# Optimization experiments

Measured on AMD Instinct MI355X. Metric: run time of the kernel, lower is better.

## Reference

```python
import jax, jax.numpy as jnp
import numpy as np

VOXEL_SIZE = jnp.array([0.075, 0.075], dtype=jnp.float32)
PC_RANGE = jnp.array([-54.0, -54.0], dtype=jnp.float32)
FUSION_STRIDE = 8.0
SRC_STRIDES = (4.0, 8.0)
RADII = (2.4, 4.8)
NSAMPLE = 16
NKEY = 500


def _mlp(x, w1, g1, b1, w2, b2):
    # Linear(no bias) + BatchNorm(eval, running mean=0/var=1 -> affine) + ReLU, then Linear
    h = jax.nn.relu((x @ w1) * g1 + b1)
    return h @ w2 + b2


def _world(coords, stride):
    # voxel coord -> world xy center
    return (coords.astype(jnp.float32) + 0.5) * stride * VOXEL_SIZE + PC_RANGE


def _gather_rows(x, idx):
    # x: (B, N, ...), idx: (B, ...) -> per-batch row gather
    return jax.vmap(lambda f, i: f[i])(x, idx)


def _knn(key_world, src_world, src_feat, radius):
    # key_world (B,Nk,2), src_world (B,Ns,2), src_feat (B,Ns,C)
    d2 = jnp.sum((key_world[:, :, None, :] - src_world[:, None, :, :]) ** 2, axis=-1)  # (B,Nk,Ns)
    d2 = jnp.where(d2 <= radius * radius, d2, jnp.inf)
    negd, idx = jax.lax.top_k(-d2, NSAMPLE)  # nearest NSAMPLE within radius, (B,Nk,K)
    valid = jnp.isfinite(negd).astype(src_feat.dtype)  # empty==0 mask
    feats = _gather_rows(src_feat, idx)  # (B,Nk,K,C)
    return feats * valid[..., None]


def setup_inputs() -> dict:
    key = jax.random.key(0)
    ks = jax.random.split(key, 24)
    s = 0.05
    return {
        'fusion_feat': jax.random.normal(ks[0], (2, 20000, 128), jnp.float32),
        'src_feat_a': jax.random.normal(ks[1], (2, 30000, 128), jnp.float32),
        'src_feat_b': jax.random.normal(ks[2], (2, 30000, 128), jnp.float32),
        'heat_w1': jax.random.normal(ks[3], (128, 128), jnp.float32) * s,
        'heat_g1': jnp.ones((128,), jnp.float32),
        'heat_b1': jnp.zeros((128,), jnp.float32),
        'heat_w2': jax.random.normal(ks[4], (128, 10), jnp.float32) * s,
        'heat_b2': jnp.zeros((10,), jnp.float32),
        'knn_w': jax.random.normal(ks[5], (2, 16), jnp.float32) * s,
        'knn_b': jnp.zeros((2,), jnp.float32),
        'kw_w1': jax.random.normal(ks[6], (128, 64), jnp.float32) * s,
        'kw_g1': jnp.ones((64,), jnp.float32),
        'kw_b1': jnp.zeros((64,), jnp.float32),
        'kw_w2': jax.random.normal(ks[7], (64, 3), jnp.float32) * s,
        'kw_b2': jnp.zeros((3,), jnp.float32),
        'fuse_w1': jax.random.normal(ks[8], (256, 256), jnp.float32) * s,
        'fuse_g1': jnp.ones((256,), jnp.float32),
        'fuse_b1': jnp.zeros((256,), jnp.float32),
        'fuse_w2': jax.random.normal(ks[9], (256, 128), jnp.float32) * s,
        'fuse_b2': jnp.zeros((128,), jnp.float32),
        'fusion_coords': jax.random.randint(ks[10], (2, 20000, 2), 0, 180, jnp.int32),
        'src_coords_a': jax.random.randint(ks[11], (2, 30000, 2), 0, 360, jnp.int32),
        'src_coords_b': jax.random.randint(ks[12], (2, 30000, 2), 0, 180, jnp.int32),
    }


def reference(fusion_feat, src_feat_a, src_feat_b, heat_w1, heat_g1, heat_b1,
              heat_w2, heat_b2, knn_w, knn_b, kw_w1, kw_g1, kw_b1, kw_w2, kw_b2,
              fuse_w1, fuse_g1, fuse_b1, fuse_w2, fuse_b2,
              fusion_coords, src_coords_a, src_coords_b):
    B = fusion_feat.shape[0]
    # heatmap head over all fusion voxels
    scores10 = _mlp(fusion_feat, heat_w1, heat_g1, heat_b1, heat_w2, heat_b2)  # (B,Nf,10)
    heat_scores = jnp.max(scores10, axis=-1)
    cls = jnp.argmax(scores10, axis=-1)
    # per-sample top-k key voxel selection
    _, tki = jax.lax.top_k(jax.nn.sigmoid(heat_scores), NKEY)  # (B,Nk)
    key_feat = _gather_rows(fusion_feat, tki)      # (B,Nk,128)
    key_coords = _gather_rows(fusion_coords, tki)  # (B,Nk,2)
    key_class = _gather_rows(cls, tki)             # (B,Nk)
    key_world = _world(key_coords, FUSION_STRIDE)  # (B,Nk,2)

    srcs = ((src_feat_a, src_coords_a), (src_feat_b, src_coords_b))
    mlp_feats = []
    for s, (sf, sc) in enumerate(srcs):
        sw = _world(sc, SRC_STRIDES[s])
        kf = _knn(key_world, sw, sf, RADII[s])  # (B,Nk,K,C), zeroed where empty
        # Linear over the K neighbor axis (knn_feat_mlp: NSAMPLE -> 1)
        mf = jnp.einsum('bnkc,k->bnc', kf, knn_w[s]) + knn_b[s]
        mlp_feats.append(mf)

    w = jax.nn.softmax(_mlp(key_feat, kw_w1, kw_g1, kw_b1, kw_w2, kw_b2), axis=-1)  # (B,Nk,3)
    # faithful to original: key_voxel_feat is re-scaled cumulatively inside the loop
    kvf = key_feat
    fuse_sum = jnp.zeros_like(key_feat)
    for i in range(len(srcs)):
        kvf = w[..., i:i + 1] * kvf
        fuse_sum = fuse_sum + kvf * mlp_feats[i]
    fused = jnp.concatenate([fuse_sum, kvf], axis=-1)  # (B,Nk,256)
    out = _mlp(fused, fuse_w1, fuse_g1, fuse_b1, fuse_w2, fuse_b2)  # (B,Nk,128)

    bs_col = jnp.broadcast_to(jnp.arange(B, dtype=key_coords.dtype)[:, None, None], (B, NKEY, 1))
    key_voxel_indices = jnp.concatenate([bs_col, key_coords], axis=-1).reshape(B * NKEY, 3)
    return (out.reshape(B * NKEY, -1), key_voxel_indices,
            heat_scores.reshape(-1), scores10.reshape(-1, scores10.shape[-1]), key_class)
```

## Files before the change

### kernel.cpp

```cpp
#include <hip/hip_runtime.h>
#include <math.h>

#define BB 2
#define NF 20000
#define NS 30000
#define CH 128
#define NK 500
#define KNN 16
#define KPB 4

#define HA 2.4024f
#define HB 4.8048f
#define NCA 45
#define NCB 23
#define CELLS_A 2025
#define CELLS_B 529

#define GB 8
#define SLICE 3750
#define SLICE4 1875

#define OUT0_OFF 0
#define OUT1_OFF 128000
#define OUT2_OFF 131000
#define OUT3_OFF 171000
#define OUT4_OFF 571000

#define WS_CLS   0
#define WS_TKI   160000
#define WS_KW    164000
#define WS_MF    172000
#define WS_KEYS  WS_MF
#define WS_BH    492000
#define WS_GSTART 1196000
#define WS_PTS    1236880
#define WS_PIDX   2196880

#define STB(s,b)  ((s) ? (4052 + (b) * 530) : ((b) * 2026))

__device__ __forceinline__ void fma4(float4& acc, float sc, const float4& wv) {
    acc.x += sc * wv.x; acc.y += sc * wv.y;
    acc.z += sc * wv.z; acc.w += sc * wv.w;
}

__device__ __forceinline__ unsigned ordf(float s) {
    unsigned u = __float_as_uint(s);
    return (u & 0x80000000u) ? ~u : (u | 0x80000000u);
}

__device__ __forceinline__ int cell_of(int cxi, int cyi, float stride, float inv_h,
                                       int nc, float& sx, float& sy)
{
    sx = __fadd_rn(__fmul_rn(__fmul_rn(__fadd_rn((float)cxi, 0.5f), stride), 0.075f), -54.0f);
    sy = __fadd_rn(__fmul_rn(__fmul_rn(__fadd_rn((float)cyi, 0.5f), stride), 0.075f), -54.0f);
    int cx = (int)floorf((sx + 54.0f) * inv_h);
    int cy = (int)floorf((sy + 54.0f) * inv_h);
    cx = min(max(cx, 0), nc - 1);
    cy = min(max(cy, 0), nc - 1);
    return cy * nc + cx;
}

__global__ __launch_bounds__(256) void heat_kernel(
    const float* __restrict__ x,
    const float* __restrict__ w1,
    const float* __restrict__ g1, const float* __restrict__ b1,
    const float* __restrict__ w2,
    const float* __restrict__ b2,
    float* __restrict__ out_heat,
    float* __restrict__ out_s10,
    int* __restrict__ cls,
    unsigned long long* __restrict__ keys,
    const int* __restrict__ sca, const int* __restrict__ scb,
    int* __restrict__ bh)
{
    __shared__ float As[64 * 76];
    __shared__ float Ws[64 * 132];
    __shared__ float W2s[1280];
    const int tid = threadIdx.x;

    if (blockIdx.x < 4 * GB) {
        const int gflat = blockIdx.x;
        const int sb = gflat >> 3;
        const int gg = gflat & (GB - 1);
        const int s = sb >> 1, b = sb & 1;
        const float stride = s ? 8.0f : 4.0f;
        const float inv_h = s ? (1.0f / HB) : (1.0f / HA);
        const int nc = s ? NCB : NCA;
        const int2* sc = ((const int2*)(s ? scb : sca)) + (size_t)b * NS;
        const int4* scv = (const int4*)sc;
        int* hist_l = (int*)As;

        for (int i = tid; i < 2048; i += 256) hist_l[i] = 0;
        __syncthreads();
        for (int p = gg * SLICE4 + tid; p < (gg + 1) * SLICE4; p += 256) {
            int4 v = scv[p];
            float sx, sy;
            int cell0 = cell_of(v.x, v.y, stride, inv_h, nc, sx, sy);
            int cell1 = cell_of(v.z, v.w, stride, inv_h, nc, sx, sy);
            atomicAdd(&hist_l[cell0], 1);
            atomicAdd(&hist_l[cell1], 1);
        }
        __syncthreads();
        int* bhp = bh + (gflat << 11);
        for (int i = tid; i < 2048; i += 256) bhp[i] = hist_l[i];
        return;
    }

    const int m0 = (blockIdx.x - 4 * GB) * 64;
    const int tx = tid & 15;
    const int ty = tid >> 4;

    for (int v = tid; v < 1280; v += 256) W2s[v] = w2[v];

    float acc[4][8];
#pragma unroll
    for (int i = 0; i < 4; ++i)
#pragma unroll
        for (int j = 0; j < 8; ++j) acc[i][j] = 0.f;

    const float4* xv = (const float4*)x;
    const float4* w1v = (const float4*)w1;

    for (int kc = 0; kc < 128; kc += 64) {
#pragma unroll
        for (int i = 0; i < 4; ++i) {
            int v = tid + i * 256;
            int row = v >> 4, c4 = v & 15;
            float4 val = xv[(size_t)(m0 + row) * 32 + (kc >> 2) + c4];
            *(float4*)&As[row * 76 + c4 * 4] = val;
        }
#pragma unroll
        for (int i = 0; i < 8; ++i) {
            int v = tid + i * 256;
            int k = v >> 5, c4 = v & 31;
            float4 val = w1v[(size_t)(kc + k) * 32 + c4];
            *(float4*)&Ws[k * 132 + c4 * 4] = val;
        }
        __syncthreads();

        const float* a0p = &As[(ty * 4 + 0) * 76];
        const float* a1p = &As[(ty * 4 + 1) * 76];
        const float* a2p = &As[(ty * 4 + 2) * 76];
        const float* a3p = &As[(ty * 4 + 3) * 76];
#pragma unroll 4
        for (int k = 0; k < 64; ++k) {
            float4 bA = *(const float4*)&Ws[k * 132 + tx * 4];
            float4 bB = *(const float4*)&Ws[k * 132 + 64 + tx * 4];
            float a0 = a0p[k], a1 = a1p[k], a2 = a2p[k], a3 = a3p[k];
            acc[0][0] += a0 * bA.x; acc[0][1] += a0 * bA.y; acc[0][2] += a0 * bA.z; acc[0][3] += a0 * bA.w;
            acc[0][4] += a0 * bB.x; acc[0][5] += a0 * bB.y; acc[0][6] += a0 * bB.z; acc[0][7] += a0 * bB.w;
            acc[1][0] += a1 * bA.x; acc[1][1] += a1 * bA.y; acc[1][2] += a1 * bA.z; acc[1][3] += a1 * bA.w;
            acc[1][4] += a1 * bB.x; acc[1][5] += a1 * bB.y; acc[1][6] += a1 * bB.z; acc[1][7] += a1 * bB.w;
            acc[2][0] += a2 * bA.x; acc[2][1] += a2 * bA.y; acc[2][2] += a2 * bA.z; acc[2][3] += a2 * bA.w;
            acc[2][4] += a2 * bB.x; acc[2][5] += a2 * bB.y; acc[2][6] += a2 * bB.z; acc[2][7] += a2 * bB.w;
            acc[3][0] += a3 * bA.x; acc[3][1] += a3 * bA.y; acc[3][2] += a3 * bA.z; acc[3][3] += a3 * bA.w;
            acc[3][4] += a3 * bB.x; acc[3][5] += a3 * bB.y; acc[3][6] += a3 * bB.z; acc[3][7] += a3 * bB.w;
        }
        __syncthreads();
    }

    float4 g1a = ((const float4*)g1)[tx], g1b = ((const float4*)g1)[16 + tx];
    float4 b1a = ((const float4*)b1)[tx], b1b = ((const float4*)b1)[16 + tx];
    float* Hs = Ws;
#pragma unroll
    for (int i = 0; i < 4; ++i) {
        int row = ty * 4 + i;
        float4 hA, hB;
        hA.x = fmaxf(acc[i][0] * g1a.x + b1a.x, 0.f);
        hA.y = fmaxf(acc[i][1] * g1a.y + b1a.y, 0.f);
        hA.z = fmaxf(acc[i][2] * g1a.z + b1a.z, 0.f);
        hA.w = fmaxf(acc[i][3] * g1a.w + b1a.w, 0.f);
        hB.x = fmaxf(acc[i][4] * g1b.x + b1b.x, 0.f);
        hB.y = fmaxf(acc[i][5] * g1b.y + b1b.y, 0.f);
        hB.z = fmaxf(acc[i][6] * g1b.z + b1b.z, 0.f);
        hB.w = fmaxf(acc[i][7] * g1b.w + b1b.w, 0.f);
        *(float4*)&Hs[row * 132 + tx * 4] = hA;
        *(float4*)&Hs[row * 132 + 64 + tx * 4] = hB;
    }
    __syncthreads();

    const int r = tid >> 2;
    const int p = tid & 3;
    float a2[10];
#pragma unroll
    for (int c = 0; c < 10; ++c) a2[c] = 0.f;
    for (int kk = 0; kk < 32; ++kk) {
        int k = kk * 4 + p;
        float hv = Hs[r * 132 + k];
#pragma unroll
        for (int c = 0; c < 10; ++c) a2[c] += hv * W2s[k * 10 + c];
    }
#pragma unroll
    for (int c = 0; c < 10; ++c) {
        a2[c] += __shfl_xor(a2[c], 1);
        a2[c] += __shfl_xor(a2[c], 2);
    }
    if (p == 0) {
        int m = m0 + r;
        float best = -INFINITY;
        int bi = 0;
#pragma unroll
        for (int c = 0; c < 10; ++c) {
            float s = a2[c] + b2[c];
            out_s10[(size_t)m * 10 + c] = s;
            if (s > best) { best = s; bi = c; }
        }
        out_heat[m] = best;
        cls[m] = bi;
        int b = m / NF;
        unsigned i = (unsigned)(m - b * NF);
        float sig = 1.0f / (1.0f + expf(-best));
        keys[m] = ((unsigned long long)ordf(sig) << 32) | (unsigned)(~i);
    }
}

#define H1BINS 16384

__global__ __launch_bounds__(1024) void mid_kernel(
    const unsigned long long* __restrict__ keys,
    const int* __restrict__ cls,
    const int* __restrict__ fcoords,
    float* __restrict__ out1,
    float* __restrict__ out4,
    int* __restrict__ tki,
    float* __restrict__ keyworld,
    const int* __restrict__ sca, const int* __restrict__ scb,
    const int* __restrict__ bh,
    int* __restrict__ gstart,
    float2* __restrict__ pts, int* __restrict__ pidx)
{
    __shared__ unsigned h[H1BINS];
    __shared__ unsigned sA[1024], sB[1024];
    __shared__ unsigned long long list[1024];
    __shared__ unsigned short bins16[NF];
    __shared__ unsigned chunk_s, aboveC_s, T1_s, aboveT1_s, cand_s, thr_s, cnt_s;
    const int tid = threadIdx.x;
    const int blk = blockIdx.x;

    if (blk >= 2) {
        const int idx = blk - 2;
        const int sb = idx >> 3;
        const int j = idx & (GB - 1);
        const int s = sb >> 1, b = sb & 1;
        const int n = s ? CELLS_B : CELLS_A;
        const int nc = s ? NCB : NCA;
        const float stride = s ? 8.0f : 4.0f;
        const float inv_h = s ? (1.0f / HB) : (1.0f / HA);
        const int stb = STB(s, b);
        const int2* sc = ((const int2*)(s ? scb : sca)) + (size_t)b * NS;
        const int4* scv = (const int4*)sc;
        const size_t pbase = ((size_t)s * BB + b) * NS;
        const int* bhsb = bh + (sb << 14);
        int* tot = (int*)h;
        int* cur = ((int*)h) + 2048;
        int* scn0 = (int*)sA;
        int* scn1 = (int*)sB;

        for (int c = tid; c < 2048; c += 1024) {
            int t = 0, pr = 0;
#pragma unroll
            for (int g = 0; g < GB; ++g) {
                int v = bhsb[(g << 11) + c];
                t += v;
                if (g < j) pr += v;
            }
            tot[c] = t;
            cur[c] = pr;
        }
        __syncthreads();
        const int i0 = tid * 2, i1 = tid * 2 + 1;
        int c0 = (i0 < n) ? tot[i0] : 0;
        int c1 = (i1 < n) ? tot[i1] : 0;
        scn0[tid] = c0 + c1;
        __syncthreads();
        int* srcp = scn0; int* dstp = scn1;
        for (int off = 1; off < 1024; off <<= 1) {
            int v = srcp[tid];
            if (tid >= off) v += srcp[tid - off];
            dstp[tid] = v;
            __syncthreads();
            int* t = srcp; srcp = dstp; dstp = t;
        }
        const int excl = (tid == 0) ? 0 : srcp[tid - 1];
        if (i0 < n) {
            if (j == 0) gstart[stb + i0] = excl;
            cur[i0] += excl;
        }
        if (i1 < n) {
            if (j == 0) gstart[stb + i1] = excl + c0;
            cur[i1] += excl + c0;
        }
        if (j == 0 && tid == 0) gstart[stb + n] = NS;
        __syncthreads();
        for (int p = j * SLICE4 + tid; p < (j + 1) * SLICE4; p += 1024) {
            int4 v = scv[p];
            float sx0, sy0, sx1, sy1;
            int cell0 = cell_of(v.x, v.y, stride, inv_h, nc, sx0, sy0);
            int cell1 = cell_of(v.z, v.w, stride, inv_h, nc, sx1, sy1);
            int pos0 = atomicAdd(&cur[cell0], 1);
            int pos1 = atomicAdd(&cur[cell1], 1);
            pts[pbase + pos0] = make_float2(sx0, sy0);
            pidx[pbase + pos0] = p * 2;
            pts[pbase + pos1] = make_float2(sx1, sy1);
            pidx[pbase + pos1] = p * 2 + 1;
        }
        return;
    }

    const int b = blk;
    const unsigned long long* kb = keys + (size_t)b * NF;
    const unsigned K = NK;

    for (int i = tid; i < H1BINS; i += 1024) h[i] = 0u;
    __syncthreads();
    for (int i2 = tid; i2 < NF / 2; i2 += 1024) {
        ulonglong2 kv = ((const ulonglong2*)kb)[i2];
        unsigned b0 = (unsigned)(kv.x >> 50);
        unsigned b1_ = (unsigned)(kv.y >> 50);
        bins16[2 * i2] = (unsigned short)b0;
        bins16[2 * i2 + 1] = (unsigned short)b1_;
        atomicAdd(&h[b0], 1u);
        atomicAdd(&h[b1_], 1u);
    }
    __syncthreads();
    unsigned ck = 0;
    {
        int base = tid * 16;
#pragma unroll
        for (int j = 0; j < 16; ++j) ck += h[base + j];
        sA[tid] = ck;
    }
    __syncthreads();
    unsigned* srcp = sA; unsigned* dstp = sB;
    for (int off = 1; off < 1024; off <<= 1) {
        unsigned v = srcp[tid];
        if (tid + off < 1024) v += srcp[tid + off];
        dstp[tid] = v;
        __syncthreads();
        unsigned* t = srcp; srcp = dstp; dstp = t;
    }
    {
        unsigned suf = srcp[tid];
        unsigned above = suf - ck;
        if (above < K && K <= suf) { chunk_s = (unsigned)tid; aboveC_s = above; }
    }
    __syncthreads();
    if (tid == 0) {
        int bin = (int)chunk_s * 16 + 15;
        unsigned acc = aboveC_s;
        for (;; --bin) { if (acc + h[bin] >= K) break; acc += h[bin]; }
        T1_s = (unsigned)bin;
        aboveT1_s = acc;
        cand_s = acc + h[bin];
        cnt_s = 0u;
    }
    __syncthreads();
    const unsigned T1 = T1_s;

    if (cand_s <= 1024u) {
        const unsigned* b32v = (const unsigned*)bins16;
        for (int i2 = tid; i2 < NF / 2; i2 += 1024) {
            unsigned pk = b32v[i2];
            if ((pk & 0xFFFFu) >= T1) {
                unsigned pos = atomicAdd(&cnt_s, 1u);
                if (pos < 1024u) list[pos] = kb[2 * i2];
            }
            if ((pk >> 16) >= T1) {
                unsigned pos = atomicAdd(&cnt_s, 1u);
                if (pos < 1024u) list[pos] = kb[2 * i2 + 1];
            }
        }
    } else {
        const unsigned K2 = K - aboveT1_s;
        h[tid] = 0u;
        __syncthreads();
#pragma unroll 4
        for (int i = tid; i < NF; i += 1024) {
            unsigned long long key = kb[i];
            if ((unsigned)(key >> 50) == T1)
                atomicAdd(&h[(unsigned)(key >> 40) & 1023u], 1u);
        }
        __syncthreads();
        unsigned hb = h[tid];
        sA[tid] = hb;
        __syncthreads();
        unsigned* s2 = sA; unsigned* d2 = sB;
        for (int off = 1; off < 1024; off <<= 1) {
            unsigned v = s2[tid];
            if (tid + off < 1024) v += s2[tid + off];
            d2[tid] = v;
            __syncthreads();
            unsigned* t = s2; s2 = d2; d2 = t;
        }
        {
            unsigned suf = s2[tid];
            unsigned above = suf - hb;
            if (above < K2 && K2 <= suf) thr_s = (T1 << 10) | (unsigned)tid;
        }
        __syncthreads();
        const unsigned thr24 = thr_s;
#pragma unroll 4
        for (int i = tid; i < NF; i += 1024) {
            unsigned long long key = kb[i];
            if ((unsigned)(key >> 40) >= thr24) {
                unsigned pos = atomicAdd(&cnt_s, 1u);
                if (pos < 1024u) list[pos] = key;
            }
        }
    }
    __syncthreads();
    const int cc = (int)(cnt_s > 1024u ? 1024u : cnt_s);

    if (tid < cc) {
        unsigned long long mykey = list[tid];
        unsigned r = 0;
#pragma unroll 8
        for (int j = 0; j < cc; ++j) r += (list[j] > mykey) ? 1u : 0u;
        if (r < (unsigned)NK) {
            int idx = (int)(~(unsigned)(mykey & 0xFFFFFFFFull));
            tki[b * NK + (int)r] = idx;
            int c0 = fcoords[((size_t)b * NF + idx) * 2 + 0];
            int c1 = fcoords[((size_t)b * NF + idx) * 2 + 1];
            size_t o = (size_t)(b * NK + (int)r);
            out1[o * 3 + 0] = (float)b;
            out1[o * 3 + 1] = (float)c0;
            out1[o * 3 + 2] = (float)c1;
            float wx = __fadd_rn(__fmul_rn(__fmul_rn(__fadd_rn((float)c0, 0.5f), 8.0f), 0.075f), -54.0f);
            float wy = __fadd_rn(__fmul_rn(__fmul_rn(__fadd_rn((float)c1, 0.5f), 8.0f), 0.075f), -54.0f);
            keyworld[o * 2 + 0] = wx;
            keyworld[o * 2 + 1] = wy;
            out4[o] = (float)cls[(size_t)b * NF + idx];
        }
    }
}

__global__ __launch_bounds__(256) void knn_kernel(
    const float* __restrict__ sfa, const float* __restrict__ sfb,
    const int* __restrict__ gstart,
    const float2* __restrict__ pts, const int* __restrict__ pidx,
    const float* __restrict__ knn_w,
    const float* __restrict__ knn_b,
    const float* __restrict__ keyworld,
    float* __restrict__ mf)
{
    __shared__ unsigned long long list[1024];
    __shared__ float psum[128];
    __shared__ unsigned cnt_s;
    const int tid = threadIdx.x;
    const int blk = blockIdx.x;
    const int s = blk / (BB * NK);
    const int rest = blk % (BB * NK);
    const int b = rest / NK;
    const int r = rest % NK;
    const float* sfeat = s ? sfb : sfa;
    const float r2 = s ? (float)(4.8 * 4.8) : (float)(2.4 * 2.4);
    const float inv_h = s ? (1.0f / HB) : (1.0f / HA);
    const int nc = s ? NCB : NCA;
    const int stb = STB(s, b);
    const size_t pbase = ((size_t)s * BB + b) * NS;

    if (tid == 0) cnt_s = 0u;
    __syncthreads();
    const float kx = keyworld[((size_t)b * NK + r) * 2 + 0];
    const float ky = keyworld[((size_t)b * NK + r) * 2 + 1];
    int cx = (int)floorf((kx + 54.0f) * inv_h);
    int cy = (int)floorf((ky + 54.0f) * inv_h);
    cx = min(max(cx, 0), nc - 1);
    cy = min(max(cy, 0), nc - 1);
    const int c0 = max(cx - 1, 0), c1 = min(cx + 1, nc - 1);
    const int cy0 = max(cy - 1, 0), cy1 = min(cy + 1, nc - 1);

    for (int cyy = cy0; cyy <= cy1; ++cyy) {
        int lo = gstart[stb + cyy * nc + c0];
        int hi = gstart[stb + cyy * nc + c1 + 1];
        for (int p = lo + tid; p < hi; p += 256) {
            float2 w = pts[pbase + p];
            float dx = __fsub_rn(kx, w.x);
            float dy = __fsub_rn(ky, w.y);
            float d2 = __fadd_rn(__fmul_rn(dx, dx), __fmul_rn(dy, dy));
            if (d2 <= r2) {
                unsigned pos = atomicAdd(&cnt_s, 1u);
                if (pos < 1024u)
                    list[pos] = ((unsigned long long)__float_as_uint(d2) << 32)
                              | (unsigned)pidx[pbase + p];
            }
        }
    }
    __syncthreads();
    int cc = (int)cnt_s;
    if (cc > 1024) cc = 1024;
    int n2 = 16;
    while (n2 < cc) n2 <<= 1;
    for (int i = tid; i < n2; i += 256)
        if (i >= cc) list[i] = ~0ull;
    __syncthreads();
    for (int kk = 2; kk <= n2; kk <<= 1) {
        for (int j = kk >> 1; j > 0; j >>= 1) {
            for (int i = tid; i < n2; i += 256) {
                int ixj = i ^ j;
                if (ixj > i) {
                    unsigned long long a = list[i], bv = list[ixj];
                    bool up = ((i & kk) == 0);
                    bool sw = up ? (a > bv) : (a < bv);
                    if (sw) { list[i] = bv; list[ixj] = a; }
                }
            }
            __syncthreads();
        }
    }
    {
        int K = cc < KNN ? cc : KNN;
        int col = tid & 127, half = tid >> 7;
        float acc = 0.f;
        int k0 = half * 8, k1 = min(K, half * 8 + 8);
        for (int k = k0; k < k1; ++k) {
            unsigned i = (unsigned)(list[k] & 0xFFFFFFFFull);
            acc += knn_w[s * 16 + k] * sfeat[((size_t)b * NS + i) * CH + col];
        }
        if (half) psum[col] = acc;
        __syncthreads();
        if (!half)
            mf[(((size_t)s * BB + b) * NK + r) * CH + col] = knn_b[s] + acc + psum[col];
    }
}

__global__ __launch_bounds__(1024) void fuse_kernel(
    const float* __restrict__ ffeat,
    const int* __restrict__ tki,
    const float* __restrict__ kw_w1, const float* __restrict__ kw_g1,
    const float* __restrict__ kw_b1, const float* __restrict__ kw_w2,
    const float* __restrict__ kw_b2,
    const float* __restrict__ fuse_w1, const float* __restrict__ fuse_g1,
    const float* __restrict__ fuse_b1, const float* __restrict__ fuse_w2,
    const float* __restrict__ fuse_b2,
    const float* __restrict__ mf,
    float* __restrict__ out0)
{
    __shared__ float pL[16384];
    __shared__ float xsT[512];
    __shared__ float mfs[1024];
    __shared__ float fusedvT[1024];
    __shared__ float h2sT[1024];
    __shared__ float prm[964];
    __shared__ float hsX[256];
    __shared__ float p2[96];
    __shared__ float l3[12];
    __shared__ float wsm[8];
    __shared__ int idxs[KPB], bs[KPB], rs[KPB];
    const int tid = threadIdx.x;
    const int f0 = blockIdx.x * KPB;

    if (tid < 964) {
        float v;
        if (tid < 64)       v = kw_g1[tid];
        else if (tid < 128) v = kw_b1[tid - 64];
        else if (tid < 320) v = kw_w2[tid - 128];
        else if (tid < 323) v = kw_b2[tid - 320];
        else if (tid < 324) v = 0.f;
        else if (tid < 580) v = fuse_g1[tid - 324];
        else if (tid < 836) v = fuse_b1[tid - 580];
        else                v = fuse_b2[tid - 836];
        prm[tid] = v;
    }
    if (tid < KPB) {
        int flat = f0 + tid;
        int b = flat / NK;
        bs[tid] = b;
        rs[tid] = flat - b * NK;
        idxs[tid] = tki[flat];
    }
    __syncthreads();

    if (tid < 128) {
        int key = tid >> 5, c4 = tid & 31;
        float4 v = ((const float4*)(ffeat + ((size_t)bs[key] * NF + idxs[key]) * CH))[c4];
        xsT[(c4 * 4 + 0) * 4 + key] = v.x;
        xsT[(c4 * 4 + 1) * 4 + key] = v.y;
        xsT[(c4 * 4 + 2) * 4 + key] = v.z;
        xsT[(c4 * 4 + 3) * 4 + key] = v.w;
    }
    if (tid < 256) {
        int ss = tid >> 7, key = (tid >> 5) & 3, c4 = tid & 31;
        float4 v = ((const float4*)(mf + (((size_t)ss * BB + bs[key]) * NK + rs[key]) * CH))[c4];
        *(float4*)&mfs[ss * 512 + key * 128 + c4 * 4] = v;
    }
    __syncthreads();

    if (tid < 256) {
        const int og = tid & 15, kseg = tid >> 4;
        float4 wr[8];
#pragma unroll
        for (int m = 0; m < 8; ++m)
            wr[m] = ((const float4*)kw_w1)[(kseg * 8 + m) * 16 + og];
        float4 a0 = {0, 0, 0, 0}, a1 = {0, 0, 0, 0}, a2 = {0, 0, 0, 0}, a3 = {0, 0, 0, 0};
#pragma unroll
        for (int m = 0; m < 8; ++m) {
            float4 f4 = *(const float4*)&xsT[(kseg * 8 + m) * 4];
            fma4(a0, f4.x, wr[m]);
            fma4(a1, f4.y, wr[m]);
            fma4(a2, f4.z, wr[m]);
            fma4(a3, f4.w, wr[m]);
        }
        *(float4*)&pL[(kseg * 4 + 0) * 64 + og * 4] = a0;
        *(float4*)&pL[(kseg * 4 + 1) * 64 + og * 4] = a1;
        *(float4*)&pL[(kseg * 4 + 2) * 64 + og * 4] = a2;
        *(float4*)&pL[(kseg * 4 + 3) * 64 + og * 4] = a3;
    }
    __syncthreads();
    if (tid < 256) {
        int out = tid >> 2, key = tid & 3;
        float s = 0.f;
#pragma unroll
        for (int ks = 0; ks < 16; ++ks) s += pL[(ks * 4 + key) * 64 + out];
        float t = s * prm[out] + prm[64 + out];
        hsX[key * 64 + out] = t > 0.f ? t : 0.f;
    }
    __syncthreads();
    if (tid < 96) {
        int key = tid / 24, rr = tid % 24, out = rr >> 3, seg = rr & 7;
        float acc = 0.f;
#pragma unroll
        for (int m = 0; m < 8; ++m) {
            int k = seg * 8 + m;
            acc += hsX[key * 64 + k] * prm[128 + k * 3 + out];
        }
        p2[(key * 3 + out) * 8 + seg] = acc;
    }
    __syncthreads();
    if (tid < 12) {
        int key = tid / 3, out = tid % 3;
        float s = 0.f;
#pragma unroll
        for (int j = 0; j < 8; ++j) s += p2[(key * 3 + out) * 8 + j];
        l3[key * 3 + out] = s + prm[320 + out];
    }
    __syncthreads();
    if (tid < KPB) {
        float l0 = l3[tid * 3], l1 = l3[tid * 3 + 1], l2 = l3[tid * 3 + 2];
        float m = fmaxf(l0, fmaxf(l1, l2));
        float e0 = expf(l0 - m), e1 = expf(l1 - m), e2 = expf(l2 - m);
        float sum = e0 + e1 + e2;
        wsm[tid * 2 + 0] = e0 / sum;
        wsm[tid * 2 + 1] = e1 / sum;
    }
    __syncthreads();

    {
        int c = tid >> 2, key = tid & 3;
        float w0 = wsm[key * 2], w1_ = wsm[key * 2 + 1];
        float val;
        if (c < 128) {
            float xv_ = xsT[c * 4 + key];
            float m0 = mfs[key * 128 + c];
            float m1 = mfs[512 + key * 128 + c];
            float kv = w0 * xv_;
            float kv2 = w1_ * kv;
            val = kv * m0 + kv2 * m1;
        } else {
            float xv_ = xsT[(c - 128) * 4 + key];
            val = w1_ * (w0 * xv_);
        }
        fusedvT[tid] = val;
    }
    __syncthreads();

    {
        const int og = tid & 63, kseg = tid >> 6;
        const float4* w1v = (const float4*)fuse_w1;
        float4 wr[16];
#pragma unroll
        for (int m = 0; m < 16; ++m)
            wr[m] = w1v[(kseg * 16 + m) * 64 + og];
        float4 a0 = {0, 0, 0, 0}, a1 = {0, 0, 0, 0}, a2 = {0, 0, 0, 0}, a3 = {0, 0, 0, 0};
#pragma unroll
        for (int m = 0; m < 16; ++m) {
            float4 f4 = *(const float4*)&fusedvT[(kseg * 16 + m) * 4];
            fma4(a0, f4.x, wr[m]);
            fma4(a1, f4.y, wr[m]);
            fma4(a2, f4.z, wr[m]);
            fma4(a3, f4.w, wr[m]);
        }
        *(float4*)&pL[(kseg * 4 + 0) * 256 + og * 4] = a0;
        *(float4*)&pL[(kseg * 4 + 1) * 256 + og * 4] = a1;
        *(float4*)&pL[(kseg * 4 + 2) * 256 + og * 4] = a2;
        *(float4*)&pL[(kseg * 4 + 3) * 256 + og * 4] = a3;
    }
    __syncthreads();
    {
        int out = tid >> 2, key = tid & 3;
        float s = 0.f;
#pragma unroll
        for (int ks = 0; ks < 16; ++ks) s += pL[(ks * 4 + key) * 256 + out];
        float t = s * prm[324 + out] + prm[580 + out];
        h2sT[out * 4 + key] = t > 0.f ? t : 0.f;
    }
    __syncthreads();

    {
        const int og2 = tid & 31, kseg2 = tid >> 5;
        const float4* w2v = (const float4*)fuse_w2;
        float4 wr[8];
#pragma unroll
        for (int m = 0; m < 8; ++m)
            wr[m] = w2v[(kseg2 * 8 + m) * 32 + og2];
        float4 a0 = {0, 0, 0, 0}, a1 = {0, 0, 0, 0}, a2 = {0, 0, 0, 0}, a3 = {0, 0, 0, 0};
#pragma unroll
        for (int m = 0; m < 8; ++m) {
            float4 f4 = *(const float4*)&h2sT[(kseg2 * 8 + m) * 4];
            fma4(a0, f4.x, wr[m]);
            fma4(a1, f4.y, wr[m]);
            fma4(a2, f4.z, wr[m]);
            fma4(a3, f4.w, wr[m]);
        }
        *(float4*)&pL[(kseg2 * 4 + 0) * 128 + og2 * 4] = a0;
        *(float4*)&pL[(kseg2 * 4 + 1) * 128 + og2 * 4] = a1;
        *(float4*)&pL[(kseg2 * 4 + 2) * 128 + og2 * 4] = a2;
        *(float4*)&pL[(kseg2 * 4 + 3) * 128 + og2 * 4] = a3;
    }
    __syncthreads();
    if (tid < 512) {
        int out = tid >> 2, key = tid & 3;
        float s = prm[836 + out];
#pragma unroll
        for (int ks = 0; ks < 32; ++ks) s += pL[(ks * 4 + key) * 128 + out];
        out0[((size_t)bs[key] * NK + rs[key]) * CH + out] = s;
    }
}

extern "C" void kernel_launch(void* const* d_in, const int* in_sizes, int n_in,
                              void* d_out, int out_size, void* d_ws, size_t ws_size,
                              hipStream_t stream)
{
    const float* fusion_feat = (const float*)d_in[0];
    const float* src_feat_a  = (const float*)d_in[1];
    const float* src_feat_b  = (const float*)d_in[2];
    const float* heat_w1 = (const float*)d_in[3];
    const float* heat_g1 = (const float*)d_in[4];
    const float* heat_b1 = (const float*)d_in[5];
    const float* heat_w2 = (const float*)d_in[6];
    const float* heat_b2 = (const float*)d_in[7];
    const float* knn_w   = (const float*)d_in[8];
    const float* knn_b   = (const float*)d_in[9];
    const float* kw_w1   = (const float*)d_in[10];
    const float* kw_g1   = (const float*)d_in[11];
    const float* kw_b1   = (const float*)d_in[12];
    const float* kw_w2   = (const float*)d_in[13];
    const float* kw_b2   = (const float*)d_in[14];
    const float* fuse_w1 = (const float*)d_in[15];
    const float* fuse_g1 = (const float*)d_in[16];
    const float* fuse_b1 = (const float*)d_in[17];
    const float* fuse_w2 = (const float*)d_in[18];
    const float* fuse_b2 = (const float*)d_in[19];
    const int* fusion_coords = (const int*)d_in[20];
    const int* src_coords_a  = (const int*)d_in[21];
    const int* src_coords_b  = (const int*)d_in[22];

    float* out = (float*)d_out;
    char* ws = (char*)d_ws;
    int* cls = (int*)(ws + WS_CLS);
    int* tki = (int*)(ws + WS_TKI);
    float* keyworld = (float*)(ws + WS_KW);
    float* mf = (float*)(ws + WS_MF);
    unsigned long long* keys = (unsigned long long*)(ws + WS_KEYS);
    int* bh = (int*)(ws + WS_BH);
    int* gstart = (int*)(ws + WS_GSTART);
    float2* pts = (float2*)(ws + WS_PTS);
    int* pidx = (int*)(ws + WS_PIDX);

    heat_kernel<<<(BB * NF) / 64 + 4 * GB, 256, 0, stream>>>(
        fusion_feat, heat_w1, heat_g1, heat_b1, heat_w2, heat_b2,
        out + OUT2_OFF, out + OUT3_OFF, cls, keys,
        src_coords_a, src_coords_b, bh);

    mid_kernel<<<2 + 4 * GB, 1024, 0, stream>>>(
        keys, cls, fusion_coords,
        out + OUT1_OFF, out + OUT4_OFF, tki, keyworld,
        src_coords_a, src_coords_b, bh, gstart, pts, pidx);

    knn_kernel<<<2 * BB * NK, 256, 0, stream>>>(
        src_feat_a, src_feat_b, gstart, pts, pidx,
        knn_w, knn_b, keyworld, mf);

    fuse_kernel<<<(BB * NK) / KPB, 1024, 0, stream>>>(
        fusion_feat, tki, kw_w1, kw_g1, kw_b1, kw_w2, kw_b2,
        fuse_w1, fuse_g1, fuse_b1, fuse_w2, fuse_b2, mf, out + OUT0_OFF);
}
```

Measured before the change: 232.3 us.

## Replace shared-memory Hillis-Steele scans with wavefront shuffle scans and shrink heat K-tile

The three 1024-thread block scans in mid_kernel previously used ten-step ping-pong shared-memory passes, each ending in a barrier. They are replaced by a helper that does an inclusive wavefront scan with shuffles and then combines the 16 wave totals through a small shared array, so only two barriers remain per scan. The suffix sums needed for top-k threshold selection are now computed from the total minus the prefix. Separately, heat_kernel's K-tile shrinks from 64 to 32 and its shared buffers are pooled, which lowers LDS use and may raise occupancy at the cost of more loop iterations and barriers.

```diff
diff --git a/kernel.cpp b/kernel.cpp
--- a/kernel.cpp
+++ b/kernel.cpp
@@ -58,6 +58,31 @@
     cx = min(max(cx, 0), nc - 1);
     cy = min(max(cy, 0), nc - 1);
     return cy * nc + cx;
+}
+
+__device__ __forceinline__ unsigned block_scan_incl(unsigned v, int tid,
+                                                    volatile unsigned* ws,
+                                                    unsigned* total)
+{
+    const int lane = tid & 63, wid = tid >> 6;
+    unsigned p = v;
+#pragma unroll
+    for (int off = 1; off < 64; off <<= 1) {
+        unsigned t = (unsigned)__shfl_up((int)p, off);
+        if (lane >= off) p += t;
+    }
+    __syncthreads();
+    if (lane == 63) ws[wid] = p;
+    __syncthreads();
+    unsigned woff = 0, tot = 0;
+#pragma unroll
+    for (int w = 0; w < 16; ++w) {
+        unsigned s = ws[w];
+        tot += s;
+        if (w < wid) woff += s;
+    }
+    *total = tot;
+    return p + woff;
 }
 
 __global__ __launch_bounds__(256) void heat_kernel(
@@ -73,8 +98,7 @@
     const int* __restrict__ sca, const int* __restrict__ scb,
     int* __restrict__ bh)
 {
-    __shared__ float As[64 * 76];
-    __shared__ float Ws[64 * 132];
+    __shared__ float Pool[8448];
     __shared__ float W2s[1280];
     const int tid = threadIdx.x;
 
@@ -88,7 +112,7 @@
         const int nc = s ? NCB : NCA;
         const int2* sc = ((const int2*)(s ? scb : sca)) + (size_t)b * NS;
         const int4* scv = (const int4*)sc;
-        int* hist_l = (int*)As;
+        int* hist_l = (int*)Pool;
 
         for (int i = tid; i < 2048; i += 256) hist_l[i] = 0;
         __syncthreads();
@@ -109,6 +133,8 @@
     const int m0 = (blockIdx.x - 4 * GB) * 64;
     const int tx = tid & 15;
     const int ty = tid >> 4;
+    float* As = Pool;
+    float* Ws = Pool + 2304;
 
     for (int v = tid; v < 1280; v += 256) W2s[v] = w2[v];
 
@@ -121,16 +147,16 @@
     const float4* xv = (const float4*)x;
     const float4* w1v = (const float4*)w1;
 
-    for (int kc = 0; kc < 128; kc += 64) {
+    for (int kc = 0; kc < 128; kc += 32) {
+#pragma unroll
+        for (int i = 0; i < 2; ++i) {
+            int v = tid + i * 256;
+            int row = v >> 3, c4 = v & 7;
+            float4 val = xv[(size_t)(m0 + row) * 32 + (kc >> 2) + c4];
+            *(float4*)&As[row * 36 + c4 * 4] = val;
+        }
 #pragma unroll
         for (int i = 0; i < 4; ++i) {
-            int v = tid + i * 256;
-            int row = v >> 4, c4 = v & 15;
-            float4 val = xv[(size_t)(m0 + row) * 32 + (kc >> 2) + c4];
-            *(float4*)&As[row * 76 + c4 * 4] = val;
-        }
-#pragma unroll
-        for (int i = 0; i < 8; ++i) {
             int v = tid + i * 256;
             int k = v >> 5, c4 = v & 31;
             float4 val = w1v[(size_t)(kc + k) * 32 + c4];
@@ -138,12 +164,12 @@
         }
         __syncthreads();
 
-        const float* a0p = &As[(ty * 4 + 0) * 76];
-        const float* a1p = &As[(ty * 4 + 1) * 76];
-        const float* a2p = &As[(ty * 4 + 2) * 76];
-        const float* a3p = &As[(ty * 4 + 3) * 76];
+        const float* a0p = &As[(ty * 4 + 0) * 36];
+        const float* a1p = &As[(ty * 4 + 1) * 36];
+        const float* a2p = &As[(ty * 4 + 2) * 36];
+        const float* a3p = &As[(ty * 4 + 3) * 36];
 #pragma unroll 4
-        for (int k = 0; k < 64; ++k) {
+        for (int k = 0; k < 32; ++k) {
             float4 bA = *(const float4*)&Ws[k * 132 + tx * 4];
             float4 bB = *(const float4*)&Ws[k * 132 + 64 + tx * 4];
             float a0 = a0p[k], a1 = a1p[k], a2 = a2p[k], a3 = a3p[k];
@@ -161,7 +187,7 @@
 
     float4 g1a = ((const float4*)g1)[tx], g1b = ((const float4*)g1)[16 + tx];
     float4 b1a = ((const float4*)b1)[tx], b1b = ((const float4*)b1)[16 + tx];
-    float* Hs = Ws;
+    float* Hs = Pool;
 #pragma unroll
     for (int i = 0; i < 4; ++i) {
         int row = ty * 4 + i;
@@ -230,9 +256,9 @@
     float2* __restrict__ pts, int* __restrict__ pidx)
 {
     __shared__ unsigned h[H1BINS];
-    __shared__ unsigned sA[1024], sB[1024];
     __shared__ unsigned long long list[1024];
     __shared__ unsigned short bins16[NF];
+    __shared__ unsigned wsum[16];
     __shared__ unsigned chunk_s, aboveC_s, T1_s, aboveT1_s, cand_s, thr_s, cnt_s;
     const int tid = threadIdx.x;
     const int blk = blockIdx.x;
@@ -253,8 +279,6 @@
         const int* bhsb = bh + (sb << 14);
         int* tot = (int*)h;
         int* cur = ((int*)h) + 2048;
-        int* scn0 = (int*)sA;
-        int* scn1 = (int*)sB;
 
         for (int c = tid; c < 2048; c += 1024) {
             int t = 0, pr = 0;
@@ -271,17 +295,9 @@
         const int i0 = tid * 2, i1 = tid * 2 + 1;
         int c0 = (i0 < n) ? tot[i0] : 0;
         int c1 = (i1 < n) ? tot[i1] : 0;
-        scn0[tid] = c0 + c1;
-        __syncthreads();
-        int* srcp = scn0; int* dstp = scn1;
-        for (int off = 1; off < 1024; off <<= 1) {
-            int v = srcp[tid];
-            if (tid >= off) v += srcp[tid - off];
-            dstp[tid] = v;
-            __syncthreads();
-            int* t = srcp; srcp = dstp; dstp = t;
-        }
-        const int excl = (tid == 0) ? 0 : srcp[tid - 1];
+        unsigned totsum;
+        unsigned P = block_scan_incl((unsigned)(c0 + c1), tid, wsum, &totsum);
+        const int excl = (int)P - (c0 + c1);
         if (i0 < n) {
             if (j == 0) gstart[stb + i0] = excl;
             cur[i0] += excl;
@@ -328,20 +344,12 @@
         int base = tid * 16;
 #pragma unroll
         for (int j = 0; j < 16; ++j) ck += h[base + j];
-        sA[tid] = ck;
-    }
-    __syncthreads();
-    unsigned* srcp = sA; unsigned* dstp = sB;
-    for (int off = 1; off < 1024; off <<= 1) {
-        unsigned v = srcp[tid];
-        if (tid + off < 1024) v += srcp[tid + off];
-        dstp[tid] = v;
-        __syncthreads();
-        unsigned* t = srcp; srcp = dstp; dstp = t;
     }
     {
-        unsigned suf = srcp[tid];
-        unsigned above = suf - ck;
+        unsigned tot;
+        unsigned P = block_scan_incl(ck, tid, wsum, &tot);
+        unsigned suf = tot - P + ck;
+        unsigned above = tot - P;
         if (above < K && K <= suf) { chunk_s = (unsigned)tid; aboveC_s = above; }
     }
     __syncthreads();
@@ -382,19 +390,11 @@
         }
         __syncthreads();
         unsigned hb = h[tid];
-        sA[tid] = hb;
-        __syncthreads();
-        unsigned* s2 = sA; unsigned* d2 = sB;
-        for (int off = 1; off < 1024; off <<= 1) {
-            unsigned v = s2[tid];
-            if (tid + off < 1024) v += s2[tid + off];
-            d2[tid] = v;
-            __syncthreads();
-            unsigned* t = s2; s2 = d2; d2 = t;
-        }
         {
-            unsigned suf = s2[tid];
-            unsigned above = suf - hb;
+            unsigned tot2;
+            unsigned P2 = block_scan_incl(hb, tid, wsum, &tot2);
+            unsigned suf = tot2 - P2 + hb;
+            unsigned above = tot2 - P2;
             if (above < K2 && K2 <= suf) thr_s = (T1 << 10) | (unsigned)tid;
         }
         __syncthreads();
```

Result: no change. 229.6 us (-1.1%).
